# Kernel optimization log

Hardware: AMD Instinct MI355X
Metric: run time of the kernel (lower is better)

Reference implementation:

```python
import jax, jax.numpy as jnp
import numpy as np

N_HEAD = 16
D_MODEL = 1024
D_HEAD = 64
SCALE = 1.0 / D_HEAD ** 0.5
LN_EPS = 1e-5


def layer_norm(x, g, b):
    mu = jnp.mean(x, axis=-1, keepdims=True)
    var = jnp.mean(jnp.square(x - mu), axis=-1, keepdims=True)
    return (x - mu) * jax.lax.rsqrt(var + LN_EPS) * g + b


def setup_inputs() -> dict:
    key = jax.random.key(0)
    ks = jax.random.split(key, 6)
    T, B = 2048, 4
    h = jax.random.normal(ks[0], (T, B, D_MODEL), dtype=jnp.float32)
    # key-padding mask, shape (klen, bsz); True = masked
    attn_mask = jax.random.randint(ks[1], (T, B), 0, 2).astype(jnp.bool_)
    s = 1.0 / np.sqrt(D_MODEL)
    wq = jax.random.uniform(ks[2], (N_HEAD * D_HEAD, D_MODEL), minval=-s, maxval=s, dtype=jnp.float32)
    wkv = jax.random.uniform(ks[3], (2 * N_HEAD * D_HEAD, D_MODEL), minval=-s, maxval=s, dtype=jnp.float32)
    wo = jax.random.uniform(ks[4], (D_MODEL, N_HEAD * D_HEAD), minval=-s, maxval=s, dtype=jnp.float32)
    ln_g = jnp.ones((D_MODEL,), jnp.float32)
    ln_b = jnp.zeros((D_MODEL,), jnp.float32)
    return {"h": h, "attn_mask": attn_mask, "wq": wq, "wkv": wkv,
            "wo": wo, "ln_g": ln_g, "ln_b": ln_b}


def reference(h, attn_mask, wq, wkv, wo, ln_g, ln_b):
    T, B, _ = h.shape
    c = h  # mems is None
    head_q = (h @ wq.T).reshape(T, B, N_HEAD, D_HEAD)
    kv = c @ wkv.T
    head_k, head_v = jnp.split(kv, 2, axis=-1)
    head_k = head_k.reshape(T, B, N_HEAD, D_HEAD)
    head_v = head_v.reshape(T, B, N_HEAD, D_HEAD)

    # scores: [qlen, klen, bsz, n_head]
    attn_score = jnp.einsum('ibnd,jbnd->ijbn', head_q, head_k) * SCALE
    attn_score = jnp.where(attn_mask[None, :, :, None], -jnp.inf, attn_score)
    attn_prob = jax.nn.softmax(attn_score, axis=1)

    attn_vec = jnp.einsum('ijbn,jbnd->ibnd', attn_prob, head_v)
    attn_vec = attn_vec.reshape(T, B, N_HEAD * D_HEAD)
    attn_out = attn_vec @ wo.T
    # post-lnorm residual (pre_lnorm=False); gate='plus' path unused here
    return layer_norm(h + attn_out, ln_g, ln_b)
```

## Files before the change

### kernel.cpp

```cpp
#include <hip/hip_runtime.h>

#define T_LEN 2048
#define BSZ 4
#define NHEAD 16
#define DHEAD 64
#define DMODEL 1024
#define SCALE 0.125f
#define L2E_SCALE (0.125f * 1.44269504f)
#define ROW 72

typedef __bf16 bf16x8 __attribute__((ext_vector_type(8)));
typedef float f32x4 __attribute__((ext_vector_type(4)));

__device__ __forceinline__ float bf2f(unsigned short u) {
  union { unsigned int i; float f; } v; v.i = ((unsigned int)u) << 16; return v.f;
}
__device__ __forceinline__ unsigned short f2bf(float f) {
  union { float f; unsigned int i; } v; v.f = f;
  unsigned int r = v.i + 0x7fffu + ((v.i >> 16) & 1u);
  return (unsigned short)(r >> 16);
}

typedef __attribute__((address_space(1))) void* gptr_t;
typedef __attribute__((address_space(3))) void* lptr_t;

__device__ __forceinline__ void load_lds16(const void* g, void* l) {
  __builtin_amdgcn_global_load_lds((gptr_t)g, (lptr_t)l, 16, 0, 0);
}

__global__ __launch_bounds__(256) void prep_kernel(const unsigned char* __restrict__ mask,
                                                   int* __restrict__ pos,
                                                   int* __restrict__ nkeys) {
  __shared__ int s_any;
  const int tid = threadIdx.x;
  if (tid == 0) s_any = 0;
  __syncthreads();
  int acc = 0;
  for (int i = tid; i < T_LEN * BSZ; i += 256)
    if ((i & 3) != 0 && mask[i] != 0) acc = 1;
  if (acc) atomicOr(&s_any, 1);
  __syncthreads();
  const int mmode = s_any ? 0 : 1;
  const int wv = tid >> 6, lane = tid & 63;
  const int b = wv;
  int run = 0;
  for (int j0 = 0; j0 < T_LEN; j0 += 64) {
    const int j = j0 + lane;
    const int mval = mmode ? ((const int*)mask)[(size_t)j * BSZ + b]
                           : (int)mask[(size_t)j * BSZ + b];
    const int keep = (mval == 0) ? 1 : 0;
    int x = keep;
#pragma unroll
    for (int off = 1; off < 64; off <<= 1) {
      const int y = __shfl_up(x, off, 64);
      if (lane >= off) x += y;
    }
    pos[b * T_LEN + j] = keep ? (run + x - keep) : -1;
    run += __shfl(x, 63, 64);
  }
  if (lane == 0) nkeys[b] = run;
}

__global__ __launch_bounds__(256) void cvt_all(const float* __restrict__ h,
                                               const float* __restrict__ wq,
                                               const float* __restrict__ wkv,
                                               const float* __restrict__ wo,
                                               unsigned short* __restrict__ h_bf,
                                               unsigned short* __restrict__ wq_bf,
                                               unsigned short* __restrict__ wkv_bf,
                                               unsigned short* __restrict__ wo_bf) {
  const size_t E4 = (size_t)T_LEN * BSZ * DMODEL / 4;
  const size_t W4 = (size_t)NHEAD * DHEAD * DMODEL / 4;
  const size_t g = (size_t)blockIdx.x * 256 + threadIdx.x;
  const float* src; unsigned short* dst; size_t off;
  if (g < E4)                { src = h;   dst = h_bf;   off = g; }
  else if (g < E4 + W4)      { src = wq;  dst = wq_bf;  off = g - E4; }
  else if (g < E4 + 3 * W4)  { src = wkv; dst = wkv_bf; off = g - E4 - W4; }
  else                       { src = wo;  dst = wo_bf;  off = g - E4 - 3 * W4; }
  const float4 v = *(const float4*)(src + off * 4);
  ushort4 o;
  o.x = f2bf(v.x); o.y = f2bf(v.y); o.z = f2bf(v.z); o.w = f2bf(v.w);
  *(ushort4*)(dst + off * 4) = o;
}

__global__ __launch_bounds__(256) void gemm_qkv(const unsigned short* __restrict__ A,
                                                const unsigned short* __restrict__ Wq,
                                                const unsigned short* __restrict__ Wkv,
                                                const int* __restrict__ pos,
                                                unsigned short* __restrict__ outQ,
                                                unsigned short* __restrict__ outK,
                                                unsigned short* __restrict__ outVt) {
  __shared__ alignas(16) unsigned short As[128 * 32];
  __shared__ alignas(16) unsigned short Bs[128 * 32];
  const int K = DMODEL;
  const int tid  = threadIdx.x;
  const int lane = tid & 63;
  const int wv   = tid >> 6;
  const int m0 = blockIdx.y * 128;
  const int n0 = blockIdx.x * 128;
  const int wr = (wv >> 1) * 64;
  const int wc = (wv & 1) * 64;
  const int mi   = lane & 15;
  const int quad = lane >> 4;

  f32x4 acc[4][4] = {};

  const int rowq = tid >> 2;
  const int kg   = (tid & 3) * 8;
  const unsigned short* Bsrc = (n0 < DMODEL) ? (Wq + (size_t)n0 * K)
                                             : (Wkv + (size_t)(n0 - DMODEL) * K);
  const unsigned short* Ag0 = A + (size_t)(m0 + rowq) * K + kg;
  const unsigned short* Ag1 = Ag0 + (size_t)64 * K;
  const unsigned short* Bg0 = Bsrc + (size_t)rowq * K + kg;
  const unsigned short* Bg1 = Bg0 + (size_t)64 * K;
  unsigned short* AsW0 = As + wv * 512;
  unsigned short* AsW1 = As + 2048 + wv * 512;
  unsigned short* BsW0 = Bs + wv * 512;
  unsigned short* BsW1 = Bs + 2048 + wv * 512;

  for (int k0 = 0; k0 < K; k0 += 32) {
    load_lds16(Ag0 + k0, AsW0);
    load_lds16(Ag1 + k0, AsW1);
    load_lds16(Bg0 + k0, BsW0);
    load_lds16(Bg1 + k0, BsW1);
    __syncthreads();
    bf16x8 af[4], bfr[4];
#pragma unroll
    for (int rt = 0; rt < 4; rt++)
      af[rt] = *(const bf16x8*)(As + (wr + rt * 16 + mi) * 32 + quad * 8);
#pragma unroll
    for (int ct = 0; ct < 4; ct++)
      bfr[ct] = *(const bf16x8*)(Bs + (wc + ct * 16 + mi) * 32 + quad * 8);
#pragma unroll
    for (int rt = 0; rt < 4; rt++)
#pragma unroll
      for (int ct = 0; ct < 4; ct++)
        acc[rt][ct] = __builtin_amdgcn_mfma_f32_16x16x32_bf16(af[rt], bfr[ct], acc[rt][ct], 0, 0, 0);
    __syncthreads();
  }

  const int region = n0 >> 10;
#pragma unroll
  for (int rt = 0; rt < 4; rt++) {
#pragma unroll
    for (int r = 0; r < 4; r++) {
      const int gm = m0 + wr + rt * 16 + quad * 4 + r;
      const int i = gm >> 2, b = gm & 3;
      int p = i;
      if (region > 0) p = pos[b * T_LEN + i];
      if (region > 0 && p < 0) continue;
#pragma unroll
      for (int ct = 0; ct < 4; ct++) {
        const int gn = n0 + wc + ct * 16 + mi;
        const int gnl = gn & (DMODEL - 1);
        const int hn = gnl >> 6, d = gnl & 63;
        const float v = acc[rt][ct][r];
        if (region == 0)
          outQ[(((size_t)b * NHEAD + hn) * T_LEN + i) * DHEAD + d] = f2bf(v * L2E_SCALE);
        else if (region == 1)
          outK[(((size_t)b * NHEAD + hn) * T_LEN + p) * DHEAD + d] = f2bf(v);
        else
          outVt[(((size_t)b * NHEAD + hn) * DHEAD + d) * T_LEN + p] = f2bf(v);
      }
    }
  }
}

__global__ __launch_bounds__(256) void gemm_out(const unsigned short* __restrict__ A,
                                                const unsigned short* __restrict__ Bw,
                                                float* __restrict__ outF) {
  __shared__ alignas(16) unsigned short As[128 * 32];
  __shared__ alignas(16) unsigned short Bs[128 * 32];
  const int K = DMODEL;
  const int tid  = threadIdx.x;
  const int lane = tid & 63;
  const int wv   = tid >> 6;
  const int m0 = blockIdx.y * 128;
  const int n0 = blockIdx.x * 128;
  const int wr = (wv >> 1) * 64;
  const int wc = (wv & 1) * 64;
  const int mi   = lane & 15;
  const int quad = lane >> 4;

  f32x4 acc[4][4] = {};

  const int rowq = tid >> 2;
  const int kg   = (tid & 3) * 8;
  const unsigned short* Ag0 = A  + (size_t)(m0 + rowq) * K + kg;
  const unsigned short* Ag1 = Ag0 + (size_t)64 * K;
  const unsigned short* Bg0 = Bw + (size_t)(n0 + rowq) * K + kg;
  const unsigned short* Bg1 = Bg0 + (size_t)64 * K;
  unsigned short* AsW0 = As + wv * 512;
  unsigned short* AsW1 = As + 2048 + wv * 512;
  unsigned short* BsW0 = Bs + wv * 512;
  unsigned short* BsW1 = Bs + 2048 + wv * 512;

  for (int k0 = 0; k0 < K; k0 += 32) {
    load_lds16(Ag0 + k0, AsW0);
    load_lds16(Ag1 + k0, AsW1);
    load_lds16(Bg0 + k0, BsW0);
    load_lds16(Bg1 + k0, BsW1);
    __syncthreads();
    bf16x8 af[4], bfr[4];
#pragma unroll
    for (int rt = 0; rt < 4; rt++)
      af[rt] = *(const bf16x8*)(As + (wr + rt * 16 + mi) * 32 + quad * 8);
#pragma unroll
    for (int ct = 0; ct < 4; ct++)
      bfr[ct] = *(const bf16x8*)(Bs + (wc + ct * 16 + mi) * 32 + quad * 8);
#pragma unroll
    for (int rt = 0; rt < 4; rt++)
#pragma unroll
      for (int ct = 0; ct < 4; ct++)
        acc[rt][ct] = __builtin_amdgcn_mfma_f32_16x16x32_bf16(af[rt], bfr[ct], acc[rt][ct], 0, 0, 0);
    __syncthreads();
  }

#pragma unroll
  for (int rt = 0; rt < 4; rt++)
#pragma unroll
    for (int ct = 0; ct < 4; ct++)
#pragma unroll
      for (int r = 0; r < 4; r++) {
        const int gm = m0 + wr + rt * 16 + quad * 4 + r;
        const int gn = n0 + wc + ct * 16 + mi;
        outF[(size_t)gm * DMODEL + gn] = acc[rt][ct][r];
      }
}

template<bool TAIL>
__device__ __forceinline__ void attn_chunk(int j0, int nk, int mi, int quad,
    const unsigned short* Ks, const unsigned short* Vts, unsigned short* PsW,
    const bf16x8 (&qb)[2][2], f32x4 (&oc)[2][4], float (&rs)[2]) {
  f32x4 sc[2][4] = {};
#pragma unroll
  for (int ct = 0; ct < 4; ct++) {
    const bf16x8 kf0 = *(const bf16x8*)(Ks + (ct * 16 + mi) * ROW + quad * 8);
    const bf16x8 kf1 = *(const bf16x8*)(Ks + (ct * 16 + mi) * ROW + 32 + quad * 8);
#pragma unroll
    for (int g = 0; g < 2; g++) {
      sc[g][ct] = __builtin_amdgcn_mfma_f32_16x16x32_bf16(kf0, qb[g][0], sc[g][ct], 0, 0, 0);
      sc[g][ct] = __builtin_amdgcn_mfma_f32_16x16x32_bf16(kf1, qb[g][1], sc[g][ct], 0, 0, 0);
    }
  }
#pragma unroll
  for (int g = 0; g < 2; g++)
#pragma unroll
    for (int ct = 0; ct < 4; ct++) {
#pragma unroll
      for (int r = 0; r < 4; r++) {
        float p = __builtin_amdgcn_exp2f(sc[g][ct][r]);
        if (TAIL && (j0 + ct * 16 + quad * 4 + r >= nk)) p = 0.f;
        rs[g] += p;
        sc[g][ct][r] = p;
      }
      union { float f; unsigned u; } c0, c1, c2, c3;
      c0.f = sc[g][ct][0]; c1.f = sc[g][ct][1]; c2.f = sc[g][ct][2]; c3.f = sc[g][ct][3];
      const unsigned pk0 = (c0.u >> 16) | (c1.u & 0xFFFF0000u);
      const unsigned pk1 = (c2.u >> 16) | (c3.u & 0xFFFF0000u);
      *(uint2*)(PsW + (g * 16 + mi) * ROW + ct * 16 + quad * 4) = make_uint2(pk0, pk1);
    }
  bf16x8 pa0[2], pa1[2];
#pragma unroll
  for (int g = 0; g < 2; g++) {
    pa0[g] = *(const bf16x8*)(PsW + (g * 16 + mi) * ROW + quad * 8);
    pa1[g] = *(const bf16x8*)(PsW + (g * 16 + mi) * ROW + 32 + quad * 8);
  }
#pragma unroll
  for (int ct = 0; ct < 4; ct++) {
    const bf16x8 vf0 = *(const bf16x8*)(Vts + (ct * 16 + mi) * ROW + quad * 8);
    const bf16x8 vf1 = *(const bf16x8*)(Vts + (ct * 16 + mi) * ROW + 32 + quad * 8);
#pragma unroll
    for (int g = 0; g < 2; g++) {
      oc[g][ct] = __builtin_amdgcn_mfma_f32_16x16x32_bf16(pa0[g], vf0, oc[g][ct], 0, 0, 0);
      oc[g][ct] = __builtin_amdgcn_mfma_f32_16x16x32_bf16(pa1[g], vf1, oc[g][ct], 0, 0, 0);
    }
  }
}

__global__ __launch_bounds__(256, 4) void attn_mfma(const unsigned short* __restrict__ Qg,
                                                    const unsigned short* __restrict__ Kg,
                                                    const unsigned short* __restrict__ Vtg,
                                                    const int* __restrict__ nkeys,
                                                    unsigned short* __restrict__ av) {
  __shared__ alignas(16) unsigned short smem[18688];
  unsigned short* Ks  = smem;
  unsigned short* Vts = smem + 4608;
  unsigned short* Qs  = smem + 9216;
  float* Ls = (float*)(smem + 18432);

  const int tid  = threadIdx.x;
  const int lane = tid & 63;
  const int wv   = tid >> 6;
  const int mi   = lane & 15;
  const int quad = lane >> 4;
  const int i0 = blockIdx.x * 128;
  const int b  = blockIdx.y;
  const int n  = blockIdx.z;
  const size_t base = ((size_t)b * NHEAD + n) * T_LEN * DHEAD;
  const int nk = nkeys[b];

  for (int it = tid; it < 1024; it += 256) {
    const int r = it >> 3, c8 = (it & 7) * 8;
    *(uint4*)(Qs + r * ROW + c8) = *(const uint4*)(Qg + base + (size_t)(i0 + r) * DHEAD + c8);
  }
  __syncthreads();
  bf16x8 qb[2][2];
#pragma unroll
  for (int g = 0; g < 2; g++) {
    qb[g][0] = *(const bf16x8*)(Qs + (wv * 32 + g * 16 + mi) * ROW + quad * 8);
    qb[g][1] = *(const bf16x8*)(Qs + (wv * 32 + g * 16 + mi) * ROW + 32 + quad * 8);
  }

  f32x4 oc[2][4] = {};
  float rs[2] = {0.f, 0.f};
  unsigned short* PsW = Qs + wv * 2304;

  const int nmain = nk & ~63;
  for (int j0 = 0; j0 < nmain; j0 += 64) {
    for (int it = tid; it < 512; it += 256) {
      const int r = it >> 3, c8 = (it & 7) * 8;
      *(uint4*)(Ks  + r * ROW + c8) = *(const uint4*)(Kg  + base + (size_t)(j0 + r) * DHEAD + c8);
      *(uint4*)(Vts + r * ROW + c8) = *(const uint4*)(Vtg + base + (size_t)r * T_LEN + j0 + c8);
    }
    __syncthreads();
    attn_chunk<false>(j0, nk, mi, quad, Ks, Vts, PsW, qb, oc, rs);
    __syncthreads();
  }
  if (nmain < nk) {
    for (int it = tid; it < 512; it += 256) {
      const int r = it >> 3, c8 = (it & 7) * 8;
      *(uint4*)(Ks  + r * ROW + c8) = *(const uint4*)(Kg  + base + (size_t)(nmain + r) * DHEAD + c8);
      *(uint4*)(Vts + r * ROW + c8) = *(const uint4*)(Vtg + base + (size_t)r * T_LEN + nmain + c8);
    }
    __syncthreads();
    attn_chunk<true>(nmain, nk, mi, quad, Ks, Vts, PsW, qb, oc, rs);
  }

#pragma unroll
  for (int g = 0; g < 2; g++) {
    float t = rs[g];
    t += __shfl_xor(t, 16, 64);
    t += __shfl_xor(t, 32, 64);
    rs[g] = t;
  }
  if (quad == 0) { Ls[wv * 32 + mi] = rs[0]; Ls[wv * 32 + 16 + mi] = rs[1]; }
  __syncthreads();
  float linv[2][4];
#pragma unroll
  for (int g = 0; g < 2; g++)
#pragma unroll
    for (int r = 0; r < 4; r++) {
      const float l = Ls[wv * 32 + g * 16 + quad * 4 + r];
      linv[g][r] = (l > 0.f) ? (1.f / l) : 0.f;
    }
#pragma unroll
  for (int g = 0; g < 2; g++)
#pragma unroll
    for (int ct = 0; ct < 4; ct++)
#pragma unroll
      for (int r = 0; r < 4; r++) {
        const int q = i0 + wv * 32 + g * 16 + quad * 4 + r;
        const int d = ct * 16 + mi;
        av[((size_t)q * BSZ + b) * DMODEL + n * DHEAD + d] = f2bf(oc[g][ct][r] * linv[g][r]);
      }
}

__global__ __launch_bounds__(256) void ln_kernel(const float* __restrict__ h,
                                                 const float* __restrict__ ao,
                                                 const float* __restrict__ g,
                                                 const float* __restrict__ bb,
                                                 float* __restrict__ out) {
  __shared__ float red[16];
  const int row = blockIdx.x;
  const int tid = threadIdx.x;
  const size_t base = (size_t)row * DMODEL;
  float x[4];
  float s = 0.f, sq = 0.f;
#pragma unroll
  for (int k = 0; k < 4; k++) {
    const int c = tid + k * 256;
    const float xv = h[base + c] + ao[base + c];
    x[k] = xv; s += xv; sq += xv * xv;
  }
#pragma unroll
  for (int off = 32; off; off >>= 1) { s += __shfl_xor(s, off, 64); sq += __shfl_xor(sq, off, 64); }
  const int wv = tid >> 6, lane = tid & 63;
  if (lane == 0) { red[wv] = s; red[8 + wv] = sq; }
  __syncthreads();
  if (tid == 0) {
    float ts = 0.f, tq = 0.f;
    for (int w = 0; w < 4; w++) { ts += red[w]; tq += red[8 + w]; }
    red[4] = ts; red[12] = tq;
  }
  __syncthreads();
  const float mu  = red[4] * (1.f / DMODEL);
  const float var = red[12] * (1.f / DMODEL) - mu * mu;
  const float inv = rsqrtf(var + 1e-5f);
#pragma unroll
  for (int k = 0; k < 4; k++) {
    const int c = tid + k * 256;
    out[base + c] = (x[k] - mu) * inv * g[c] + bb[c];
  }
}

extern "C" void kernel_launch(void* const* d_in, const int* in_sizes, int n_in,
                              void* d_out, int out_size, void* d_ws, size_t ws_size,
                              hipStream_t stream) {
  (void)in_sizes; (void)n_in; (void)out_size; (void)ws_size;
  const float* h           = (const float*)d_in[0];
  const unsigned char* msk = (const unsigned char*)d_in[1];
  const float* wq          = (const float*)d_in[2];
  const float* wkv         = (const float*)d_in[3];
  const float* wo          = (const float*)d_in[4];
  const float* lng         = (const float*)d_in[5];
  const float* lnb         = (const float*)d_in[6];
  float* out = (float*)d_out;

  const size_t E  = (size_t)T_LEN * BSZ * DMODEL;
  const size_t WQ = (size_t)NHEAD * DHEAD * DMODEL;
  char* ws = (char*)d_ws;
  int* nkeys            = (int*)ws;                       ws += 16;
  int* pos              = (int*)ws;                       ws += (size_t)BSZ * T_LEN * 4;
  unsigned short* h_bf  = (unsigned short*)ws;            ws += E * 2;
  unsigned short* wq_bf = (unsigned short*)ws;            ws += WQ * 2;
  unsigned short* wkv_bf= (unsigned short*)ws;            ws += 2 * WQ * 2;
  unsigned short* wo_bf = (unsigned short*)ws;            ws += WQ * 2;
  unsigned short* Qb    = (unsigned short*)ws;            ws += E * 2;
  unsigned short* Kb    = (unsigned short*)ws;            ws += E * 2;
  unsigned short* Vtb   = (unsigned short*)ws;            ws += E * 2;
  unsigned short* AV    = (unsigned short*)ws;            ws += E * 2;
  float* AO             = (float*)ws;

  const dim3 blk(256);
  prep_kernel<<<1, blk, 0, stream>>>(msk, pos, nkeys);
  cvt_all<<<dim3(12288), blk, 0, stream>>>(h, wq, wkv, wo, h_bf, wq_bf, wkv_bf, wo_bf);
  gemm_qkv<<<dim3(3 * DMODEL / 128, T_LEN * BSZ / 128), blk, 0, stream>>>(
      h_bf, wq_bf, wkv_bf, pos, Qb, Kb, Vtb);
  attn_mfma<<<dim3(T_LEN / 128, BSZ, NHEAD), blk, 0, stream>>>(Qb, Kb, Vtb, nkeys, AV);
  gemm_out<<<dim3(DMODEL / 128, T_LEN * BSZ / 128), blk, 0, stream>>>(AV, wo_bf, AO);
  ln_kernel<<<dim3(T_LEN * BSZ), blk, 0, stream>>>(h, AO, lng, lnb, out);
}
```

Before: 341.6 us.

## Widen GEMM K-tile to 64 with XOR-swizzled LDS, fuse prep kernels, bf16 attn output

```diff
diff --git a/kernel.cpp b/kernel.cpp
--- a/kernel.cpp
+++ b/kernel.cpp
@@ -28,11 +28,34 @@
   __builtin_amdgcn_global_load_lds((gptr_t)g, (lptr_t)l, 16, 0, 0);
 }
 
-__global__ __launch_bounds__(256) void prep_kernel(const unsigned char* __restrict__ mask,
-                                                   int* __restrict__ pos,
-                                                   int* __restrict__ nkeys) {
+__global__ __launch_bounds__(256) void cvt_prep(const float* __restrict__ h,
+                                                const float* __restrict__ wq,
+                                                const float* __restrict__ wkv,
+                                                const float* __restrict__ wo,
+                                                const unsigned char* __restrict__ mask,
+                                                unsigned short* __restrict__ h_bf,
+                                                unsigned short* __restrict__ wq_bf,
+                                                unsigned short* __restrict__ wkv_bf,
+                                                unsigned short* __restrict__ wo_bf,
+                                                int* __restrict__ pos,
+                                                int* __restrict__ nkeys) {
+  const int tid = threadIdx.x;
+  if (blockIdx.x < 12288) {
+    const size_t E4 = (size_t)T_LEN * BSZ * DMODEL / 4;
+    const size_t W4 = (size_t)NHEAD * DHEAD * DMODEL / 4;
+    const size_t g = (size_t)blockIdx.x * 256 + tid;
+    const float* src; unsigned short* dst; size_t off;
+    if (g < E4)                { src = h;   dst = h_bf;   off = g; }
+    else if (g < E4 + W4)      { src = wq;  dst = wq_bf;  off = g - E4; }
+    else if (g < E4 + 3 * W4)  { src = wkv; dst = wkv_bf; off = g - E4 - W4; }
+    else                       { src = wo;  dst = wo_bf;  off = g - E4 - 3 * W4; }
+    const float4 v = *(const float4*)(src + off * 4);
+    ushort4 o;
+    o.x = f2bf(v.x); o.y = f2bf(v.y); o.z = f2bf(v.z); o.w = f2bf(v.w);
+    *(ushort4*)(dst + off * 4) = o;
+    return;
+  }
   __shared__ int s_any;
-  const int tid = threadIdx.x;
   if (tid == 0) s_any = 0;
   __syncthreads();
   int acc = 0;
@@ -61,27 +84,48 @@
   if (lane == 0) nkeys[b] = run;
 }
 
-__global__ __launch_bounds__(256) void cvt_all(const float* __restrict__ h,
-                                               const float* __restrict__ wq,
-                                               const float* __restrict__ wkv,
-                                               const float* __restrict__ wo,
-                                               unsigned short* __restrict__ h_bf,
-                                               unsigned short* __restrict__ wq_bf,
-                                               unsigned short* __restrict__ wkv_bf,
-                                               unsigned short* __restrict__ wo_bf) {
-  const size_t E4 = (size_t)T_LEN * BSZ * DMODEL / 4;
-  const size_t W4 = (size_t)NHEAD * DHEAD * DMODEL / 4;
-  const size_t g = (size_t)blockIdx.x * 256 + threadIdx.x;
-  const float* src; unsigned short* dst; size_t off;
-  if (g < E4)                { src = h;   dst = h_bf;   off = g; }
-  else if (g < E4 + W4)      { src = wq;  dst = wq_bf;  off = g - E4; }
-  else if (g < E4 + 3 * W4)  { src = wkv; dst = wkv_bf; off = g - E4 - W4; }
-  else                       { src = wo;  dst = wo_bf;  off = g - E4 - 3 * W4; }
-  const float4 v = *(const float4*)(src + off * 4);
-  ushort4 o;
-  o.x = f2bf(v.x); o.y = f2bf(v.y); o.z = f2bf(v.z); o.w = f2bf(v.w);
-  *(ushort4*)(dst + off * 4) = o;
-}
+#define GEMM64_BODY(Aptr, Bptr)                                                        \
+  const int tid  = threadIdx.x;                                                        \
+  const int lane = tid & 63;                                                           \
+  const int wv   = tid >> 6;                                                           \
+  const int wr = (wv >> 1) * 64;                                                       \
+  const int wc = (wv & 1) * 64;                                                        \
+  const int mi   = lane & 15;                                                          \
+  const int quad = lane >> 4;                                                          \
+  f32x4 acc[4][4] = {};                                                                \
+  int rowc[4], colc[4];                                                                \
+  _Pragma("unroll")                                                                    \
+  for (int c = 0; c < 4; c++) {                                                        \
+    const int s = c * 256 + tid;                                                       \
+    rowc[c] = s >> 3;                                                                  \
+    colc[c] = ((s & 7) ^ (rowc[c] & 7)) * 8;                                           \
+  }                                                                                    \
+  const int swz = mi & 7;                                                              \
+  for (int k0 = 0; k0 < DMODEL; k0 += 64) {                                            \
+    _Pragma("unroll")                                                                  \
+    for (int c = 0; c < 4; c++) {                                                      \
+      load_lds16(Aptr + (size_t)rowc[c] * DMODEL + k0 + colc[c], As + c * 2048 + wv * 512); \
+      load_lds16(Bptr + (size_t)rowc[c] * DMODEL + k0 + colc[c], Bs + c * 2048 + wv * 512); \
+    }                                                                                  \
+    __syncthreads();                                                                   \
+    _Pragma("unroll")                                                                  \
+    for (int kq = 0; kq < 2; kq++) {                                                   \
+      const int cp = ((kq * 4 + quad) ^ swz) * 8;                                      \
+      bf16x8 af[4], bfr[4];                                                            \
+      _Pragma("unroll")                                                                \
+      for (int rt = 0; rt < 4; rt++)                                                   \
+        af[rt] = *(const bf16x8*)(As + (wr + rt * 16 + mi) * 64 + cp);                 \
+      _Pragma("unroll")                                                                \
+      for (int ct = 0; ct < 4; ct++)                                                   \
+        bfr[ct] = *(const bf16x8*)(Bs + (wc + ct * 16 + mi) * 64 + cp);                \
+      _Pragma("unroll")                                                                \
+      for (int rt = 0; rt < 4; rt++)                                                   \
+        _Pragma("unroll")                                                              \
+        for (int ct = 0; ct < 4; ct++)                                                 \
+          acc[rt][ct] = __builtin_amdgcn_mfma_f32_16x16x32_bf16(af[rt], bfr[ct], acc[rt][ct], 0, 0, 0); \
+    }                                                                                  \
+    __syncthreads();                                                                   \
+  }
 
 __global__ __launch_bounds__(256) void gemm_qkv(const unsigned short* __restrict__ A,
                                                 const unsigned short* __restrict__ Wq,
@@ -90,54 +134,14 @@
                                                 unsigned short* __restrict__ outQ,
                                                 unsigned short* __restrict__ outK,
                                                 unsigned short* __restrict__ outVt) {
-  __shared__ alignas(16) unsigned short As[128 * 32];
-  __shared__ alignas(16) unsigned short Bs[128 * 32];
-  const int K = DMODEL;
-  const int tid  = threadIdx.x;
-  const int lane = tid & 63;
-  const int wv   = tid >> 6;
+  __shared__ alignas(16) unsigned short As[128 * 64];
+  __shared__ alignas(16) unsigned short Bs[128 * 64];
   const int m0 = blockIdx.y * 128;
   const int n0 = blockIdx.x * 128;
-  const int wr = (wv >> 1) * 64;
-  const int wc = (wv & 1) * 64;
-  const int mi   = lane & 15;
-  const int quad = lane >> 4;
-
-  f32x4 acc[4][4] = {};
-
-  const int rowq = tid >> 2;
-  const int kg   = (tid & 3) * 8;
-  const unsigned short* Bsrc = (n0 < DMODEL) ? (Wq + (size_t)n0 * K)
-                                             : (Wkv + (size_t)(n0 - DMODEL) * K);
-  const unsigned short* Ag0 = A + (size_t)(m0 + rowq) * K + kg;
-  const unsigned short* Ag1 = Ag0 + (size_t)64 * K;
-  const unsigned short* Bg0 = Bsrc + (size_t)rowq * K + kg;
-  const unsigned short* Bg1 = Bg0 + (size_t)64 * K;
-  unsigned short* AsW0 = As + wv * 512;
-  unsigned short* AsW1 = As + 2048 + wv * 512;
-  unsigned short* BsW0 = Bs + wv * 512;
-  unsigned short* BsW1 = Bs + 2048 + wv * 512;
-
-  for (int k0 = 0; k0 < K; k0 += 32) {
-    load_lds16(Ag0 + k0, AsW0);
-    load_lds16(Ag1 + k0, AsW1);
-    load_lds16(Bg0 + k0, BsW0);
-    load_lds16(Bg1 + k0, BsW1);
-    __syncthreads();
-    bf16x8 af[4], bfr[4];
-#pragma unroll
-    for (int rt = 0; rt < 4; rt++)
-      af[rt] = *(const bf16x8*)(As + (wr + rt * 16 + mi) * 32 + quad * 8);
-#pragma unroll
-    for (int ct = 0; ct < 4; ct++)
-      bfr[ct] = *(const bf16x8*)(Bs + (wc + ct * 16 + mi) * 32 + quad * 8);
-#pragma unroll
-    for (int rt = 0; rt < 4; rt++)
-#pragma unroll
-      for (int ct = 0; ct < 4; ct++)
-        acc[rt][ct] = __builtin_amdgcn_mfma_f32_16x16x32_bf16(af[rt], bfr[ct], acc[rt][ct], 0, 0, 0);
-    __syncthreads();
-  }
+  const unsigned short* Abase = A + (size_t)m0 * DMODEL;
+  const unsigned short* Bbase = (n0 < DMODEL) ? (Wq + (size_t)n0 * DMODEL)
+                                              : (Wkv + (size_t)(n0 - DMODEL) * DMODEL);
+  GEMM64_BODY(Abase, Bbase)
 
   const int region = n0 >> 10;
 #pragma unroll
@@ -168,53 +172,14 @@
 
 __global__ __launch_bounds__(256) void gemm_out(const unsigned short* __restrict__ A,
                                                 const unsigned short* __restrict__ Bw,
-                                                float* __restrict__ outF) {
-  __shared__ alignas(16) unsigned short As[128 * 32];
-  __shared__ alignas(16) unsigned short Bs[128 * 32];
-  const int K = DMODEL;
-  const int tid  = threadIdx.x;
-  const int lane = tid & 63;
-  const int wv   = tid >> 6;
+                                                unsigned short* __restrict__ outB) {
+  __shared__ alignas(16) unsigned short As[128 * 64];
+  __shared__ alignas(16) unsigned short Bs[128 * 64];
   const int m0 = blockIdx.y * 128;
   const int n0 = blockIdx.x * 128;
-  const int wr = (wv >> 1) * 64;
-  const int wc = (wv & 1) * 64;
-  const int mi   = lane & 15;
-  const int quad = lane >> 4;
-
-  f32x4 acc[4][4] = {};
-
-  const int rowq = tid >> 2;
-  const int kg   = (tid & 3) * 8;
-  const unsigned short* Ag0 = A  + (size_t)(m0 + rowq) * K + kg;
-  const unsigned short* Ag1 = Ag0 + (size_t)64 * K;
-  const unsigned short* Bg0 = Bw + (size_t)(n0 + rowq) * K + kg;
-  const unsigned short* Bg1 = Bg0 + (size_t)64 * K;
-  unsigned short* AsW0 = As + wv * 512;
-  unsigned short* AsW1 = As + 2048 + wv * 512;
-  unsigned short* BsW0 = Bs + wv * 512;
-  unsigned short* BsW1 = Bs + 2048 + wv * 512;
-
-  for (int k0 = 0; k0 < K; k0 += 32) {
-    load_lds16(Ag0 + k0, AsW0);
-    load_lds16(Ag1 + k0, AsW1);
-    load_lds16(Bg0 + k0, BsW0);
-    load_lds16(Bg1 + k0, BsW1);
-    __syncthreads();
-    bf16x8 af[4], bfr[4];
-#pragma unroll
-    for (int rt = 0; rt < 4; rt++)
-      af[rt] = *(const bf16x8*)(As + (wr + rt * 16 + mi) * 32 + quad * 8);
-#pragma unroll
-    for (int ct = 0; ct < 4; ct++)
-      bfr[ct] = *(const bf16x8*)(Bs + (wc + ct * 16 + mi) * 32 + quad * 8);
-#pragma unroll
-    for (int rt = 0; rt < 4; rt++)
-#pragma unroll
-      for (int ct = 0; ct < 4; ct++)
-        acc[rt][ct] = __builtin_amdgcn_mfma_f32_16x16x32_bf16(af[rt], bfr[ct], acc[rt][ct], 0, 0, 0);
-    __syncthreads();
-  }
+  const unsigned short* Abase = A  + (size_t)m0 * DMODEL;
+  const unsigned short* Bbase = Bw + (size_t)n0 * DMODEL;
+  GEMM64_BODY(Abase, Bbase)
 
 #pragma unroll
   for (int rt = 0; rt < 4; rt++)
@@ -224,7 +189,7 @@
       for (int r = 0; r < 4; r++) {
         const int gm = m0 + wr + rt * 16 + quad * 4 + r;
         const int gn = n0 + wc + ct * 16 + mi;
-        outF[(size_t)gm * DMODEL + gn] = acc[rt][ct][r];
+        outB[(size_t)gm * DMODEL + gn] = f2bf(acc[rt][ct][r]);
       }
 }
 
@@ -367,7 +332,7 @@
 }
 
 __global__ __launch_bounds__(256) void ln_kernel(const float* __restrict__ h,
-                                                 const float* __restrict__ ao,
+                                                 const unsigned short* __restrict__ ao,
                                                  const float* __restrict__ g,
                                                  const float* __restrict__ bb,
                                                  float* __restrict__ out) {
@@ -380,7 +345,7 @@
 #pragma unroll
   for (int k = 0; k < 4; k++) {
     const int c = tid + k * 256;
-    const float xv = h[base + c] + ao[base + c];
+    const float xv = h[base + c] + bf2f(ao[base + c]);
     x[k] = xv; s += xv; sq += xv * xv;
   }
 #pragma unroll
@@ -430,11 +395,11 @@
   unsigned short* Kb    = (unsigned short*)ws;            ws += E * 2;
   unsigned short* Vtb   = (unsigned short*)ws;            ws += E * 2;
   unsigned short* AV    = (unsigned short*)ws;            ws += E * 2;
-  float* AO             = (float*)ws;
+  unsigned short* AO    = (unsigned short*)ws;
 
   const dim3 blk(256);
-  prep_kernel<<<1, blk, 0, stream>>>(msk, pos, nkeys);
-  cvt_all<<<dim3(12288), blk, 0, stream>>>(h, wq, wkv, wo, h_bf, wq_bf, wkv_bf, wo_bf);
+  cvt_prep<<<dim3(12289), blk, 0, stream>>>(h, wq, wkv, wo, msk,
+                                            h_bf, wq_bf, wkv_bf, wo_bf, pos, nkeys);
   gemm_qkv<<<dim3(3 * DMODEL / 128, T_LEN * BSZ / 128), blk, 0, stream>>>(
       h_bf, wq_bf, wkv_bf, pos, Qb, Kb, Vtb);
   attn_mfma<<<dim3(T_LEN / 128, BSZ, NHEAD), blk, 0, stream>>>(Qb, Kb, Vtb, nkeys, AV);
```

Measured after the change: 319.9 us. 1.07x faster.

## Enlarge GEMM tiles with swizzled LDS, fuse prep into convert, bf16 attn output

Applied to the files above, without the earlier changes.

```diff
diff --git a/kernel.cpp b/kernel.cpp
--- a/kernel.cpp
+++ b/kernel.cpp
@@ -28,11 +28,34 @@
   __builtin_amdgcn_global_load_lds((gptr_t)g, (lptr_t)l, 16, 0, 0);
 }
 
-__global__ __launch_bounds__(256) void prep_kernel(const unsigned char* __restrict__ mask,
-                                                   int* __restrict__ pos,
-                                                   int* __restrict__ nkeys) {
+__global__ __launch_bounds__(256) void cvt_prep(const float* __restrict__ h,
+                                                const float* __restrict__ wq,
+                                                const float* __restrict__ wkv,
+                                                const float* __restrict__ wo,
+                                                const unsigned char* __restrict__ mask,
+                                                unsigned short* __restrict__ h_bf,
+                                                unsigned short* __restrict__ wq_bf,
+                                                unsigned short* __restrict__ wkv_bf,
+                                                unsigned short* __restrict__ wo_bf,
+                                                int* __restrict__ pos,
+                                                int* __restrict__ nkeys) {
+  const int tid = threadIdx.x;
+  if (blockIdx.x < 12288) {
+    const size_t E4 = (size_t)T_LEN * BSZ * DMODEL / 4;
+    const size_t W4 = (size_t)NHEAD * DHEAD * DMODEL / 4;
+    const size_t g = (size_t)blockIdx.x * 256 + tid;
+    const float* src; unsigned short* dst; size_t off;
+    if (g < E4)                { src = h;   dst = h_bf;   off = g; }
+    else if (g < E4 + W4)      { src = wq;  dst = wq_bf;  off = g - E4; }
+    else if (g < E4 + 3 * W4)  { src = wkv; dst = wkv_bf; off = g - E4 - W4; }
+    else                       { src = wo;  dst = wo_bf;  off = g - E4 - 3 * W4; }
+    const float4 v = *(const float4*)(src + off * 4);
+    ushort4 o;
+    o.x = f2bf(v.x); o.y = f2bf(v.y); o.z = f2bf(v.z); o.w = f2bf(v.w);
+    *(ushort4*)(dst + off * 4) = o;
+    return;
+  }
   __shared__ int s_any;
-  const int tid = threadIdx.x;
   if (tid == 0) s_any = 0;
   __syncthreads();
   int acc = 0;
@@ -61,28 +84,6 @@
   if (lane == 0) nkeys[b] = run;
 }
 
-__global__ __launch_bounds__(256) void cvt_all(const float* __restrict__ h,
-                                               const float* __restrict__ wq,
-                                               const float* __restrict__ wkv,
-                                               const float* __restrict__ wo,
-                                               unsigned short* __restrict__ h_bf,
-                                               unsigned short* __restrict__ wq_bf,
-                                               unsigned short* __restrict__ wkv_bf,
-                                               unsigned short* __restrict__ wo_bf) {
-  const size_t E4 = (size_t)T_LEN * BSZ * DMODEL / 4;
-  const size_t W4 = (size_t)NHEAD * DHEAD * DMODEL / 4;
-  const size_t g = (size_t)blockIdx.x * 256 + threadIdx.x;
-  const float* src; unsigned short* dst; size_t off;
-  if (g < E4)                { src = h;   dst = h_bf;   off = g; }
-  else if (g < E4 + W4)      { src = wq;  dst = wq_bf;  off = g - E4; }
-  else if (g < E4 + 3 * W4)  { src = wkv; dst = wkv_bf; off = g - E4 - W4; }
-  else                       { src = wo;  dst = wo_bf;  off = g - E4 - 3 * W4; }
-  const float4 v = *(const float4*)(src + off * 4);
-  ushort4 o;
-  o.x = f2bf(v.x); o.y = f2bf(v.y); o.z = f2bf(v.z); o.w = f2bf(v.w);
-  *(ushort4*)(dst + off * 4) = o;
-}
-
 __global__ __launch_bounds__(256) void gemm_qkv(const unsigned short* __restrict__ A,
                                                 const unsigned short* __restrict__ Wq,
                                                 const unsigned short* __restrict__ Wkv,
@@ -90,68 +91,76 @@
                                                 unsigned short* __restrict__ outQ,
                                                 unsigned short* __restrict__ outK,
                                                 unsigned short* __restrict__ outVt) {
-  __shared__ alignas(16) unsigned short As[128 * 32];
-  __shared__ alignas(16) unsigned short Bs[128 * 32];
-  const int K = DMODEL;
+  __shared__ alignas(16) unsigned short As[256 * 64];
+  __shared__ alignas(16) unsigned short Bs[128 * 64];
   const int tid  = threadIdx.x;
   const int lane = tid & 63;
   const int wv   = tid >> 6;
-  const int m0 = blockIdx.y * 128;
+  const int m0 = blockIdx.y * 256;
   const int n0 = blockIdx.x * 128;
-  const int wr = (wv >> 1) * 64;
-  const int wc = (wv & 1) * 64;
+  const int wrow = (wv >> 1) * 128;
+  const int wcol = (wv & 1) * 64;
   const int mi   = lane & 15;
   const int quad = lane >> 4;
 
-  f32x4 acc[4][4] = {};
-
-  const int rowq = tid >> 2;
-  const int kg   = (tid & 3) * 8;
-  const unsigned short* Bsrc = (n0 < DMODEL) ? (Wq + (size_t)n0 * K)
-                                             : (Wkv + (size_t)(n0 - DMODEL) * K);
-  const unsigned short* Ag0 = A + (size_t)(m0 + rowq) * K + kg;
-  const unsigned short* Ag1 = Ag0 + (size_t)64 * K;
-  const unsigned short* Bg0 = Bsrc + (size_t)rowq * K + kg;
-  const unsigned short* Bg1 = Bg0 + (size_t)64 * K;
-  unsigned short* AsW0 = As + wv * 512;
-  unsigned short* AsW1 = As + 2048 + wv * 512;
-  unsigned short* BsW0 = Bs + wv * 512;
-  unsigned short* BsW1 = Bs + 2048 + wv * 512;
-
-  for (int k0 = 0; k0 < K; k0 += 32) {
-    load_lds16(Ag0 + k0, AsW0);
-    load_lds16(Ag1 + k0, AsW1);
-    load_lds16(Bg0 + k0, BsW0);
-    load_lds16(Bg1 + k0, BsW1);
-    __syncthreads();
-    bf16x8 af[4], bfr[4];
-#pragma unroll
-    for (int rt = 0; rt < 4; rt++)
-      af[rt] = *(const bf16x8*)(As + (wr + rt * 16 + mi) * 32 + quad * 8);
-#pragma unroll
-    for (int ct = 0; ct < 4; ct++)
-      bfr[ct] = *(const bf16x8*)(Bs + (wc + ct * 16 + mi) * 32 + quad * 8);
-#pragma unroll
-    for (int rt = 0; rt < 4; rt++)
+  const unsigned short* Abase = A + (size_t)m0 * DMODEL;
+  const unsigned short* Bbase = (n0 < DMODEL) ? (Wq + (size_t)n0 * DMODEL)
+                                              : (Wkv + (size_t)(n0 - DMODEL) * DMODEL);
+  f32x4 acc[8][4] = {};
+
+  int arow[8], acol[8], brow[4], bcol[4];
+#pragma unroll
+  for (int c = 0; c < 8; c++) {
+    const int s = c * 256 + tid;
+    arow[c] = s >> 3; acol[c] = ((s & 7) ^ (arow[c] & 7)) * 8;
+  }
+#pragma unroll
+  for (int c = 0; c < 4; c++) {
+    const int s = c * 256 + tid;
+    brow[c] = s >> 3; bcol[c] = ((s & 7) ^ (brow[c] & 7)) * 8;
+  }
+  const int swz = mi & 7;
+
+  for (int k0 = 0; k0 < DMODEL; k0 += 64) {
+#pragma unroll
+    for (int c = 0; c < 8; c++)
+      load_lds16(Abase + (size_t)arow[c] * DMODEL + k0 + acol[c], As + c * 2048 + wv * 512);
+#pragma unroll
+    for (int c = 0; c < 4; c++)
+      load_lds16(Bbase + (size_t)brow[c] * DMODEL + k0 + bcol[c], Bs + c * 2048 + wv * 512);
+    __syncthreads();
+#pragma unroll
+    for (int kq = 0; kq < 2; kq++) {
+      const int cp = ((kq * 4 + quad) ^ swz) * 8;
+      bf16x8 af[8], bfr[4];
+#pragma unroll
+      for (int rt = 0; rt < 8; rt++)
+        af[rt] = *(const bf16x8*)(As + (wrow + rt * 16 + mi) * 64 + cp);
 #pragma unroll
       for (int ct = 0; ct < 4; ct++)
-        acc[rt][ct] = __builtin_amdgcn_mfma_f32_16x16x32_bf16(af[rt], bfr[ct], acc[rt][ct], 0, 0, 0);
+        bfr[ct] = *(const bf16x8*)(Bs + (wcol + ct * 16 + mi) * 64 + cp);
+#pragma unroll
+      for (int rt = 0; rt < 8; rt++)
+#pragma unroll
+        for (int ct = 0; ct < 4; ct++)
+          acc[rt][ct] = __builtin_amdgcn_mfma_f32_16x16x32_bf16(af[rt], bfr[ct], acc[rt][ct], 0, 0, 0);
+    }
     __syncthreads();
   }
 
   const int region = n0 >> 10;
 #pragma unroll
-  for (int rt = 0; rt < 4; rt++) {
+  for (int rt = 0; rt < 8; rt++) {
 #pragma unroll
     for (int r = 0; r < 4; r++) {
-      const int gm = m0 + wr + rt * 16 + quad * 4 + r;
+      const int gm = m0 + wrow + rt * 16 + quad * 4 + r;
       const int i = gm >> 2, b = gm & 3;
       int p = i;
       if (region > 0) p = pos[b * T_LEN + i];
       if (region > 0 && p < 0) continue;
 #pragma unroll
       for (int ct = 0; ct < 4; ct++) {
-        const int gn = n0 + wc + ct * 16 + mi;
+        const int gn = n0 + wcol + ct * 16 + mi;
         const int gnl = gn & (DMODEL - 1);
         const int hn = gnl >> 6, d = gnl & 63;
         const float v = acc[rt][ct][r];
@@ -168,10 +177,9 @@
 
 __global__ __launch_bounds__(256) void gemm_out(const unsigned short* __restrict__ A,
                                                 const unsigned short* __restrict__ Bw,
-                                                float* __restrict__ outF) {
-  __shared__ alignas(16) unsigned short As[128 * 32];
-  __shared__ alignas(16) unsigned short Bs[128 * 32];
-  const int K = DMODEL;
+                                                unsigned short* __restrict__ outB) {
+  __shared__ alignas(16) unsigned short As[128 * 64];
+  __shared__ alignas(16) unsigned short Bs[128 * 64];
   const int tid  = threadIdx.x;
   const int lane = tid & 63;
   const int wv   = tid >> 6;
@@ -181,38 +189,41 @@
   const int wc = (wv & 1) * 64;
   const int mi   = lane & 15;
   const int quad = lane >> 4;
+  const unsigned short* Abase = A  + (size_t)m0 * DMODEL;
+  const unsigned short* Bbase = Bw + (size_t)n0 * DMODEL;
 
   f32x4 acc[4][4] = {};
-
-  const int rowq = tid >> 2;
-  const int kg   = (tid & 3) * 8;
-  const unsigned short* Ag0 = A  + (size_t)(m0 + rowq) * K + kg;
-  const unsigned short* Ag1 = Ag0 + (size_t)64 * K;
-  const unsigned short* Bg0 = Bw + (size_t)(n0 + rowq) * K + kg;
-  const unsigned short* Bg1 = Bg0 + (size_t)64 * K;
-  unsigned short* AsW0 = As + wv * 512;
-  unsigned short* AsW1 = As + 2048 + wv * 512;
-  unsigned short* BsW0 = Bs + wv * 512;
-  unsigned short* BsW1 = Bs + 2048 + wv * 512;
-
-  for (int k0 = 0; k0 < K; k0 += 32) {
-    load_lds16(Ag0 + k0, AsW0);
-    load_lds16(Ag1 + k0, AsW1);
-    load_lds16(Bg0 + k0, BsW0);
-    load_lds16(Bg1 + k0, BsW1);
-    __syncthreads();
-    bf16x8 af[4], bfr[4];
-#pragma unroll
-    for (int rt = 0; rt < 4; rt++)
-      af[rt] = *(const bf16x8*)(As + (wr + rt * 16 + mi) * 32 + quad * 8);
-#pragma unroll
-    for (int ct = 0; ct < 4; ct++)
-      bfr[ct] = *(const bf16x8*)(Bs + (wc + ct * 16 + mi) * 32 + quad * 8);
-#pragma unroll
-    for (int rt = 0; rt < 4; rt++)
+  int rowc[4], colc[4];
+#pragma unroll
+  for (int c = 0; c < 4; c++) {
+    const int s = c * 256 + tid;
+    rowc[c] = s >> 3;
+    colc[c] = ((s & 7) ^ (rowc[c] & 7)) * 8;
+  }
+  const int swz = mi & 7;
+  for (int k0 = 0; k0 < DMODEL; k0 += 64) {
+#pragma unroll
+    for (int c = 0; c < 4; c++) {
+      load_lds16(Abase + (size_t)rowc[c] * DMODEL + k0 + colc[c], As + c * 2048 + wv * 512);
+      load_lds16(Bbase + (size_t)rowc[c] * DMODEL + k0 + colc[c], Bs + c * 2048 + wv * 512);
+    }
+    __syncthreads();
+#pragma unroll
+    for (int kq = 0; kq < 2; kq++) {
+      const int cp = ((kq * 4 + quad) ^ swz) * 8;
+      bf16x8 af[4], bfr[4];
+#pragma unroll
+      for (int rt = 0; rt < 4; rt++)
+        af[rt] = *(const bf16x8*)(As + (wr + rt * 16 + mi) * 64 + cp);
 #pragma unroll
       for (int ct = 0; ct < 4; ct++)
-        acc[rt][ct] = __builtin_amdgcn_mfma_f32_16x16x32_bf16(af[rt], bfr[ct], acc[rt][ct], 0, 0, 0);
+        bfr[ct] = *(const bf16x8*)(Bs + (wc + ct * 16 + mi) * 64 + cp);
+#pragma unroll
+      for (int rt = 0; rt < 4; rt++)
+#pragma unroll
+        for (int ct = 0; ct < 4; ct++)
+          acc[rt][ct] = __builtin_amdgcn_mfma_f32_16x16x32_bf16(af[rt], bfr[ct], acc[rt][ct], 0, 0, 0);
+    }
     __syncthreads();
   }
 
@@ -224,7 +235,7 @@
       for (int r = 0; r < 4; r++) {
         const int gm = m0 + wr + rt * 16 + quad * 4 + r;
         const int gn = n0 + wc + ct * 16 + mi;
-        outF[(size_t)gm * DMODEL + gn] = acc[rt][ct][r];
+        outB[(size_t)gm * DMODEL + gn] = f2bf(acc[rt][ct][r]);
       }
 }
 
@@ -367,7 +378,7 @@
 }
 
 __global__ __launch_bounds__(256) void ln_kernel(const float* __restrict__ h,
-                                                 const float* __restrict__ ao,
+                                                 const unsigned short* __restrict__ ao,
                                                  const float* __restrict__ g,
                                                  const float* __restrict__ bb,
                                                  float* __restrict__ out) {
@@ -375,14 +386,13 @@
   const int row = blockIdx.x;
   const int tid = threadIdx.x;
   const size_t base = (size_t)row * DMODEL;
-  float x[4];
+  const int c = tid * 4;
+  const float4 hv = *(const float4*)(h + base + c);
+  const ushort4 a4 = *(const ushort4*)(ao + base + c);
+  float x[4] = { hv.x + bf2f(a4.x), hv.y + bf2f(a4.y), hv.z + bf2f(a4.z), hv.w + bf2f(a4.w) };
   float s = 0.f, sq = 0.f;
 #pragma unroll
-  for (int k = 0; k < 4; k++) {
-    const int c = tid + k * 256;
-    const float xv = h[base + c] + ao[base + c];
-    x[k] = xv; s += xv; sq += xv * xv;
-  }
+  for (int k = 0; k < 4; k++) { s += x[k]; sq += x[k] * x[k]; }
 #pragma unroll
   for (int off = 32; off; off >>= 1) { s += __shfl_xor(s, off, 64); sq += __shfl_xor(sq, off, 64); }
   const int wv = tid >> 6, lane = tid & 63;
@@ -397,11 +407,14 @@
   const float mu  = red[4] * (1.f / DMODEL);
   const float var = red[12] * (1.f / DMODEL) - mu * mu;
   const float inv = rsqrtf(var + 1e-5f);
-#pragma unroll
-  for (int k = 0; k < 4; k++) {
-    const int c = tid + k * 256;
-    out[base + c] = (x[k] - mu) * inv * g[c] + bb[c];
-  }
+  const float4 gv = *(const float4*)(g + c);
+  const float4 bv = *(const float4*)(bb + c);
+  float4 o;
+  o.x = (x[0] - mu) * inv * gv.x + bv.x;
+  o.y = (x[1] - mu) * inv * gv.y + bv.y;
+  o.z = (x[2] - mu) * inv * gv.z + bv.z;
+  o.w = (x[3] - mu) * inv * gv.w + bv.w;
+  *(float4*)(out + base + c) = o;
 }
 
 extern "C" void kernel_launch(void* const* d_in, const int* in_sizes, int n_in,
@@ -430,12 +443,12 @@
   unsigned short* Kb    = (unsigned short*)ws;            ws += E * 2;
   unsigned short* Vtb   = (unsigned short*)ws;            ws += E * 2;
   unsigned short* AV    = (unsigned short*)ws;            ws += E * 2;
-  float* AO             = (float*)ws;
+  unsigned short* AO    = (unsigned short*)ws;
 
   const dim3 blk(256);
-  prep_kernel<<<1, blk, 0, stream>>>(msk, pos, nkeys);
-  cvt_all<<<dim3(12288), blk, 0, stream>>>(h, wq, wkv, wo, h_bf, wq_bf, wkv_bf, wo_bf);
-  gemm_qkv<<<dim3(3 * DMODEL / 128, T_LEN * BSZ / 128), blk, 0, stream>>>(
+  cvt_prep<<<dim3(12289), blk, 0, stream>>>(h, wq, wkv, wo, msk,
+                                            h_bf, wq_bf, wkv_bf, wo_bf, pos, nkeys);
+  gemm_qkv<<<dim3(3 * DMODEL / 128, T_LEN * BSZ / 256), blk, 0, stream>>>(
       h_bf, wq_bf, wkv_bf, pos, Qb, Kb, Vtb);
   attn_mfma<<<dim3(T_LEN / 128, BSZ, NHEAD), blk, 0, stream>>>(Qb, Kb, Vtb, nkeys, AV);
   gemm_out<<<dim3(DMODEL / 128, T_LEN * BSZ / 128), blk, 0, stream>>>(AV, wo_bf, AO);
```

New measurement: 362.0 us. 6.0% more time.
